# Kernel tuning notes

Measured on AMD Instinct MI355X. Metric: run time of the kernel, lower is better.

Reference implementation:

```python
import jax, jax.numpy as jnp
import numpy as np

EPS = 1e-16  # PyG softmax denominator epsilon


def segment_softmax(alpha, batch, num_segments):
    # alpha: (n,1); softmax within each bag (PyG-style: subtract segment max)
    m = jax.ops.segment_max(alpha, batch, num_segments=num_segments)
    e = jnp.exp(alpha - m[batch])
    s = jax.ops.segment_sum(e, batch, num_segments=num_segments)
    return e / (s[batch] + EPS)


def global_softmax_pooling(x, alpha, batch, num_segments):
    a = segment_softmax(alpha, batch, num_segments)
    return jax.ops.segment_sum(x * a, batch, num_segments=num_segments)  # (B,d)


def setup_inputs() -> dict:
    key = jax.random.key(0)
    k1, k2 = jax.random.split(key)
    n, d, B = 262144, 256, 512
    x = jax.random.normal(k1, (n, d), dtype=jnp.float32)
    batch = jnp.sort(jax.random.randint(k2, (n,), 0, B))
    return {"x": x, "batch": batch, "num_segments": B}


def reference(x, batch, num_segments):
    K = 3  # module default k
    alpha = jnp.zeros((x.shape[0], 1), dtype=x.dtype)
    for _ in range(K):  # small fixed iteration count
        z = global_softmax_pooling(x, alpha, batch, num_segments)  # (B,d)
        energy = jnp.sum(z * z, axis=1, keepdims=True)  # (B,1)
        z_squashed = jnp.sqrt(energy) / (1.0 + energy) * z  # (B,d)
        # alpha_i += <x_i, z_squashed[batch_i]> (vectorizes the per-bag mm loop)
        alpha = alpha + jnp.sum(x * z_squashed[batch], axis=1, keepdims=True)
    return global_softmax_pooling(x, alpha, batch, num_segments)
```

## Files before the change

### kernel.cpp

```cpp
#include <hip/hip_runtime.h>

#define BLOCK 1024
#define D 256
#define NW 16
#define ALPHA_CAP 4096

__global__ __launch_bounds__(BLOCK, 2)
void dynpool_kernel(const float* __restrict__ x,
                    const int* __restrict__ batch,
                    float* __restrict__ out,
                    int n)
{
    __shared__ float alpha_s[ALPHA_CAP];
    __shared__ float zpart[NW][D];
    __shared__ float mw_s[NW], sw_s[NW];
    __shared__ float fct[NW + 1];
    __shared__ float red2[NW + 1];
    __shared__ float zs[D];
    __shared__ int bounds[2];

    const int tid  = threadIdx.x;
    const int s    = blockIdx.x;
    const int wv   = tid >> 6;
    const int lane = tid & 63;

    if (tid == 0) {
        int lo = 0, hi = n;
        while (lo < hi) { int mid = (lo + hi) >> 1; if (batch[mid] < s) lo = mid + 1; else hi = mid; }
        bounds[0] = lo;
        int lo2 = lo, hi2 = n;
        while (lo2 < hi2) { int mid = (lo2 + hi2) >> 1; if (batch[mid] < s + 1) lo2 = mid + 1; else hi2 = mid; }
        bounds[1] = lo2;
    }
    __syncthreads();
    const int start = bounds[0];
    const int cnt   = bounds[1] - bounds[0];

    if (cnt == 0) {
        if (tid < D) out[(size_t)s * D + tid] = 0.f;
        return;
    }

    for (int r = tid; r < cnt; r += BLOCK) alpha_s[r] = 0.f;

    float zr[4] = {0.f, 0.f, 0.f, 0.f};
    __syncthreads();

    for (int iter = 0; iter < 4; ++iter) {
        float m_run = -INFINITY, s_run = 0.f;
        float za[4] = {0.f, 0.f, 0.f, 0.f};
        for (int r = wv; r < cnt; r += NW) {
            const float4 v = *(const float4*)(x + ((size_t)(start + r)) * D + lane * 4);
            float dt = v.x * zr[0] + v.y * zr[1] + v.z * zr[2] + v.w * zr[3];
#pragma unroll
            for (int off = 32; off; off >>= 1) dt += __shfl_xor(dt, off);
            const float a_new = alpha_s[r] + dt;
            if (lane == 0) alpha_s[r] = a_new;
            const float mn = fmaxf(m_run, a_new);
            const float sc = __expf(m_run - mn);
            const float w  = __expf(a_new - mn);
            s_run = s_run * sc + w;
            za[0] = za[0] * sc + w * v.x;
            za[1] = za[1] * sc + w * v.y;
            za[2] = za[2] * sc + w * v.z;
            za[3] = za[3] * sc + w * v.w;
            m_run = mn;
        }

        if (lane == 0) { mw_s[wv] = m_run; sw_s[wv] = s_run; }
#pragma unroll
        for (int j = 0; j < 4; ++j) zpart[wv][lane * 4 + j] = za[j];
        __syncthreads();

        if (tid == 0) {
            float mg = -INFINITY;
            for (int h = 0; h < NW; ++h) mg = fmaxf(mg, mw_s[h]);
            float st = 0.f;
            for (int h = 0; h < NW; ++h) {
                const float f = __expf(mw_s[h] - mg);
                fct[h] = f;
                st += sw_s[h] * f;
            }
            fct[NW] = 1.f / (st + 1e-16f);
        }
        __syncthreads();

        float zc = 0.f;
        if (tid < D) {
#pragma unroll
            for (int h = 0; h < NW; ++h) zc += zpart[h][tid] * fct[h];
            zc *= fct[NW];
        }

        if (iter == 3) {
            if (tid < D) out[(size_t)s * D + tid] = zc;
            break;
        }

        float e = (tid < D) ? zc * zc : 0.f;
#pragma unroll
        for (int off = 32; off; off >>= 1) e += __shfl_xor(e, off);
        if (lane == 0) red2[wv] = e;
        __syncthreads();
        if (tid == 0) {
            float E = 0.f;
            for (int h = 0; h < NW; ++h) E += red2[h];
            red2[NW] = (E > 0.f) ? (sqrtf(E) / (1.f + E)) : 0.f;
        }
        __syncthreads();
        const float scale = red2[NW];
        if (tid < D) zs[tid] = zc * scale;
        __syncthreads();
#pragma unroll
        for (int j = 0; j < 4; ++j) zr[j] = zs[lane * 4 + j];
    }
}

extern "C" void kernel_launch(void* const* d_in, const int* in_sizes, int n_in,
                              void* d_out, int out_size, void* d_ws, size_t ws_size,
                              hipStream_t stream) {
    const float* x   = (const float*)d_in[0];
    const int* batch = (const int*)d_in[1];
    float* out       = (float*)d_out;
    const int n = in_sizes[1];
    const int B = out_size / D;
    dynpool_kernel<<<B, BLOCK, 0, stream>>>(x, batch, out, n);
}
```

Baseline: 159.5 us.

## Cache x as bf16 in workspace and specialize first uniform-softmax pass

Result: slower. 224.4 us (+40.6%).

```diff
diff --git a/kernel.cpp b/kernel.cpp
--- a/kernel.cpp
+++ b/kernel.cpp
@@ -5,8 +5,17 @@
 #define NW 16
 #define ALPHA_CAP 4096
 
+__device__ __forceinline__ unsigned bfbits(float f) {
+    unsigned u = __float_as_uint(f);
+    return (u + 0x7fffu + ((u >> 16) & 1u)) >> 16;
+}
+__device__ __forceinline__ float bflo(unsigned u) { return __uint_as_float(u << 16); }
+__device__ __forceinline__ float bfhi(unsigned u) { return __uint_as_float(u & 0xffff0000u); }
+
+template<int USE_WS>
 __global__ __launch_bounds__(BLOCK, 2)
 void dynpool_kernel(const float* __restrict__ x,
+                    unsigned short* __restrict__ xb,
                     const int* __restrict__ batch,
                     float* __restrict__ out,
                     int n)
@@ -47,24 +56,50 @@
     __syncthreads();
 
     for (int iter = 0; iter < 4; ++iter) {
-        float m_run = -INFINITY, s_run = 0.f;
+        float m_run, s_run = 0.f;
         float za[4] = {0.f, 0.f, 0.f, 0.f};
-        for (int r = wv; r < cnt; r += NW) {
-            const float4 v = *(const float4*)(x + ((size_t)(start + r)) * D + lane * 4);
-            float dt = v.x * zr[0] + v.y * zr[1] + v.z * zr[2] + v.w * zr[3];
+
+        if (iter == 0) {
+            m_run = 0.f;
+            for (int r = wv; r < cnt; r += NW) {
+                const size_t off = (size_t)(start + r) * D + lane * 4;
+                const float4 v = *(const float4*)(x + off);
+                if (USE_WS) {
+                    uint2 p;
+                    p.x = bfbits(v.x) | (bfbits(v.y) << 16);
+                    p.y = bfbits(v.z) | (bfbits(v.w) << 16);
+                    *(uint2*)(xb + off) = p;
+                }
+                s_run += 1.f;
+                za[0] += v.x; za[1] += v.y; za[2] += v.z; za[3] += v.w;
+            }
+        } else {
+            m_run = -INFINITY;
+            for (int r = wv; r < cnt; r += NW) {
+                const size_t off = (size_t)(start + r) * D + lane * 4;
+                float4 v;
+                if (USE_WS) {
+                    const uint2 u = *(const uint2*)(xb + off);
+                    v.x = bflo(u.x); v.y = bfhi(u.x);
+                    v.z = bflo(u.y); v.w = bfhi(u.y);
+                } else {
+                    v = *(const float4*)(x + off);
+                }
+                float dt = v.x * zr[0] + v.y * zr[1] + v.z * zr[2] + v.w * zr[3];
 #pragma unroll
-            for (int off = 32; off; off >>= 1) dt += __shfl_xor(dt, off);
-            const float a_new = alpha_s[r] + dt;
-            if (lane == 0) alpha_s[r] = a_new;
-            const float mn = fmaxf(m_run, a_new);
-            const float sc = __expf(m_run - mn);
-            const float w  = __expf(a_new - mn);
-            s_run = s_run * sc + w;
-            za[0] = za[0] * sc + w * v.x;
-            za[1] = za[1] * sc + w * v.y;
-            za[2] = za[2] * sc + w * v.z;
-            za[3] = za[3] * sc + w * v.w;
-            m_run = mn;
+                for (int o = 32; o; o >>= 1) dt += __shfl_xor(dt, o);
+                const float a_new = alpha_s[r] + dt;
+                if (lane == 0) alpha_s[r] = a_new;
+                const float mn = fmaxf(m_run, a_new);
+                const float sc = __expf(m_run - mn);
+                const float w  = __expf(a_new - mn);
+                s_run = s_run * sc + w;
+                za[0] = za[0] * sc + w * v.x;
+                za[1] = za[1] * sc + w * v.y;
+                za[2] = za[2] * sc + w * v.z;
+                za[3] = za[3] * sc + w * v.w;
+                m_run = mn;
+            }
         }
 
         if (lane == 0) { mw_s[wv] = m_run; sw_s[wv] = s_run; }
@@ -99,7 +134,7 @@
 
         float e = (tid < D) ? zc * zc : 0.f;
 #pragma unroll
-        for (int off = 32; off; off >>= 1) e += __shfl_xor(e, off);
+        for (int o = 32; o; o >>= 1) e += __shfl_xor(e, o);
         if (lane == 0) red2[wv] = e;
         __syncthreads();
         if (tid == 0) {
@@ -124,5 +159,10 @@
     float* out       = (float*)d_out;
     const int n = in_sizes[1];
     const int B = out_size / D;
-    dynpool_kernel<<<B, BLOCK, 0, stream>>>(x, batch, out, n);
+    const size_t need = (size_t)n * D * sizeof(unsigned short);
+    if (ws_size >= need) {
+        dynpool_kernel<1><<<B, BLOCK, 0, stream>>>(x, (unsigned short*)d_ws, batch, out, n);
+    } else {
+        dynpool_kernel<0><<<B, BLOCK, 0, stream>>>(x, (unsigned short*)d_ws, batch, out, n);
+    }
 }
```
